# Kernel tuning notes

Hardware: AMD Instinct MI355X
Metric: run time of the kernel (lower is better)

The kernel has to match this reference:

```python
import jax, jax.numpy as jnp
import numpy as np

M = 512          # n_clusters
D_PER = 32       # examples per cluster
FEAT = 1024      # embedding dim
ALPHA = 1.0
N_CLASSES = 128
EPS = 1e-8


def setup_inputs() -> dict:
    key = jax.random.key(0)
    k1, k2 = jax.random.split(key)
    N = M * D_PER
    inp = jax.random.normal(k1, (N, FEAT), dtype=jnp.float32)
    # class label per cluster, repeated d times so each contiguous chunk shares a class
    cluster_classes = jax.random.randint(k2, (M,), 0, N_CLASSES, dtype=jnp.int32)
    target = jnp.repeat(cluster_classes, D_PER)
    return {"input": inp, "target": target}


def reference(input, target):
    N, feat = input.shape
    m, d = M, D_PER
    # cluster assignment: sorted arange(m) repeated d times == repeat(arange(m), d)
    clusters = jnp.repeat(jnp.arange(m), d)                      # [N]
    cluster_classes = target[0 : m * d : d]                      # [m]

    # segment mean over contiguous equal-size chunks (== torch.chunk + mean + stack)
    means = input.reshape(m, d, feat).mean(axis=1)               # [m, feat]

    r2 = jnp.sum(input * input, axis=1, keepdims=True)           # [N,1]
    c2 = jnp.sum(means * means, axis=1)                          # [m]
    sample_costs = r2 + c2[None, :] - 2.0 * (input @ means.T)    # [N, m]

    # distance of each example to its own cluster mean
    intra = jnp.take_along_axis(sample_costs, clusters[:, None], axis=1)[:, 0]  # [N]

    variance = jnp.sum(intra) / float(N - 1)
    var_norm = -1.0 / (2.0 * variance ** 2)

    numerator = jnp.exp(var_norm * intra - ALPHA)                # [N]

    diff_class_mask = (target[:, None] != cluster_classes[None, :]).astype(input.dtype)  # [N,m]
    denominator = jnp.sum(diff_class_mask * jnp.exp(var_norm * sample_costs), axis=1)    # [N]

    losses = jax.nn.relu(-jnp.log(numerator / (denominator + EPS) + EPS))
    total_loss = jnp.mean(losses)

    pred = jnp.argmin(sample_costs, axis=1)                      # [N]
    acc = jnp.mean((pred == clusters).astype(jnp.float32))
    return total_loss, losses, pred, acc
```

## Files before the change

kernel.cpp:

```cpp
#include <hip/hip_runtime.h>
#include <math.h>

#define NCLUST 512
#define DPER 32
#define NFEAT 1024
#define NSAMP (NCLUST * DPER)
#define ALPHA_C 1.0f
#define EPS_C 1e-8f
#define MARGIN_C 0.25f

#define GBM 128
#define GBN 128
#define GBK 64
#define NCHUNK 8

typedef __attribute__((ext_vector_type(4))) float f32x4;
typedef __attribute__((ext_vector_type(8))) _Float16 f16x8;

__device__ __forceinline__ unsigned f2h(float f) {
  _Float16 h = (_Float16)f;
  return (unsigned)__builtin_bit_cast(ushort, h);
}

__device__ __forceinline__ void gload16(const ushort* g, ushort* l) {
  __builtin_amdgcn_global_load_lds(
      (const __attribute__((address_space(1))) unsigned int*)g,
      (__attribute__((address_space(3))) unsigned int*)l, 16, 0, 0);
}

__global__ __launch_bounds__(256) void k_pre(const float* __restrict__ inp,
                                             const int* __restrict__ target,
                                             float* __restrict__ means,
                                             ushort* __restrict__ Bf16,
                                             ushort* __restrict__ Af16,
                                             float* __restrict__ c2,
                                             float* __restrict__ r2g,
                                             float* __restrict__ percl,
                                             int* __restrict__ ccls,
                                             int* __restrict__ wcount) {
  const int m = blockIdx.x;
  const int t = threadIdx.x;
  const int w = t >> 6, l = t & 63;
  __shared__ float ldsm[4][NFEAT];
  __shared__ float red4[4];
  __shared__ float redi[4];

  const float* rowbase = inp + (size_t)m * DPER * NFEAT;
  ushort* arowbase = Af16 + (size_t)m * DPER * NFEAT;

  float4 macc0 = {0,0,0,0}, macc1 = {0,0,0,0}, macc2 = {0,0,0,0}, macc3 = {0,0,0,0};
  float r2keep[8];

  #pragma unroll 2
  for (int rr = 0; rr < 8; ++rr) {
    const int d = w * 8 + rr;
    const float* rp = rowbase + (size_t)d * NFEAT + l * 4;
    const float4 v0 = *(const float4*)(rp);
    const float4 v1 = *(const float4*)(rp + 256);
    const float4 v2 = *(const float4*)(rp + 512);
    const float4 v3 = *(const float4*)(rp + 768);
    ushort* ap = arowbase + (size_t)d * NFEAT + l * 4;
    uint2 h;
    h.x = f2h(v0.x) | (f2h(v0.y) << 16); h.y = f2h(v0.z) | (f2h(v0.w) << 16);
    *(uint2*)(ap) = h;
    h.x = f2h(v1.x) | (f2h(v1.y) << 16); h.y = f2h(v1.z) | (f2h(v1.w) << 16);
    *(uint2*)(ap + 256) = h;
    h.x = f2h(v2.x) | (f2h(v2.y) << 16); h.y = f2h(v2.z) | (f2h(v2.w) << 16);
    *(uint2*)(ap + 512) = h;
    h.x = f2h(v3.x) | (f2h(v3.y) << 16); h.y = f2h(v3.z) | (f2h(v3.w) << 16);
    *(uint2*)(ap + 768) = h;
    macc0.x += v0.x; macc0.y += v0.y; macc0.z += v0.z; macc0.w += v0.w;
    macc1.x += v1.x; macc1.y += v1.y; macc1.z += v1.z; macc1.w += v1.w;
    macc2.x += v2.x; macc2.y += v2.y; macc2.z += v2.z; macc2.w += v2.w;
    macc3.x += v3.x; macc3.y += v3.y; macc3.z += v3.z; macc3.w += v3.w;
    float p = v0.x*v0.x + v0.y*v0.y + v0.z*v0.z + v0.w*v0.w
            + v1.x*v1.x + v1.y*v1.y + v1.z*v1.z + v1.w*v1.w
            + v2.x*v2.x + v2.y*v2.y + v2.z*v2.z + v2.w*v2.w
            + v3.x*v3.x + v3.y*v3.y + v3.z*v3.z + v3.w*v3.w;
    #pragma unroll
    for (int off = 32; off; off >>= 1) p += __shfl_down(p, off);
    r2keep[rr] = p;
  }
  if (l == 0) {
    float r2s = 0.f;
    #pragma unroll
    for (int rr = 0; rr < 8; ++rr) {
      r2g[m * DPER + w * 8 + rr] = r2keep[rr];
      r2s += r2keep[rr];
    }
    redi[w] = r2s;
  }
  *(float4*)&ldsm[w][0 * 256 + l * 4] = macc0;
  *(float4*)&ldsm[w][1 * 256 + l * 4] = macc1;
  *(float4*)&ldsm[w][2 * 256 + l * 4] = macc2;
  *(float4*)&ldsm[w][3 * 256 + l * 4] = macc3;
  __syncthreads();
  float4 s0 = *(const float4*)&ldsm[0][t * 4];
  float4 s1 = *(const float4*)&ldsm[1][t * 4];
  float4 s2 = *(const float4*)&ldsm[2][t * 4];
  float4 s3 = *(const float4*)&ldsm[3][t * 4];
  const float inv = 1.0f / 32.0f;
  float4 mn;
  mn.x = (s0.x + s1.x + s2.x + s3.x) * inv;
  mn.y = (s0.y + s1.y + s2.y + s3.y) * inv;
  mn.z = (s0.z + s1.z + s2.z + s3.z) * inv;
  mn.w = (s0.w + s1.w + s2.w + s3.w) * inv;
  *(float4*)(means + (size_t)m * NFEAT + t * 4) = mn;
  uint2 bw;
  bw.x = f2h(mn.x) | (f2h(mn.y) << 16);
  bw.y = f2h(mn.z) | (f2h(mn.w) << 16);
  *(uint2*)&Bf16[(size_t)m * NFEAT + t * 4] = bw;
  float sq = mn.x * mn.x + mn.y * mn.y + mn.z * mn.z + mn.w * mn.w;
  #pragma unroll
  for (int off = 32; off; off >>= 1) sq += __shfl_down(sq, off);
  if (l == 0) red4[w] = sq;
  __syncthreads();
  if (t == 0) {
    const float cc = red4[0] + red4[1] + red4[2] + red4[3];
    c2[m] = cc;
    ccls[m] = target[m * DPER];
    percl[m] = (redi[0] + redi[1] + redi[2] + redi[3]) - 32.0f * cc;
    if (m == 0) *wcount = 0;
  }
}

__global__ __launch_bounds__(256, 2) void k_gemm(
    const ushort* __restrict__ Af16, const ushort* __restrict__ Bf16,
    const float* __restrict__ c2, const float* __restrict__ r2,
    const float* __restrict__ percl, const int* __restrict__ ccls,
    const int* __restrict__ target,
    float* __restrict__ den_p, float* __restrict__ minv_p,
    float* __restrict__ minv2_p, float* __restrict__ minc_p,
    float* __restrict__ intra_g) {
  __shared__ ushort As[2][GBM * GBK];
  __shared__ ushort Bs[2][GBN * GBK];
  __shared__ float redv[4];
  const int t = threadIdx.x;
  const int l = t & 63, w = t >> 6;
  const int wg = (blockIdx.x & 7) * 64 + (blockIdx.x >> 3);
  const int rowblk = wg >> 2, colblk = wg & 3;
  const int row0 = rowblk * GBM, c0 = colblk * GBN;
  const int wr = w >> 1, wc = w & 1;

  const int sR = l >> 3;
  const int sg = (l & 7) ^ sR;
  const ushort* sA = Af16 + (size_t)(row0 + w * 32 + sR) * NFEAT + sg * 8;
  const ushort* sB = Bf16 + (size_t)(c0 + w * 32 + sR) * NFEAT + sg * 8;

  const int fr = l & 15, fq = l >> 4;
  const int swz = fr & 7;

  f32x4 acc[4][4];
  #pragma unroll
  for (int i = 0; i < 4; ++i)
    #pragma unroll
    for (int j = 0; j < 4; ++j) acc[i][j] = (f32x4){0.f, 0.f, 0.f, 0.f};

#define STAGE(bi, ks) do {                                                   \
    _Pragma("unroll") for (int i = 0; i < 4; ++i)                            \
      gload16(sA + (size_t)i * 8 * NFEAT + (ks) * GBK,                       \
              &As[bi][(w * 32 + i * 8) * GBK]);                              \
    _Pragma("unroll") for (int i = 0; i < 4; ++i)                            \
      gload16(sB + (size_t)i * 8 * NFEAT + (ks) * GBK,                       \
              &Bs[bi][(w * 32 + i * 8) * GBK]);                              \
  } while (0)

#define COMPUTE(bi) do {                                                     \
    _Pragma("unroll") for (int kg = 0; kg < 2; ++kg) {                       \
      const int ch = (((kg * 4 + fq) ^ swz) * 8);                            \
      f16x8 a[4], b[4];                                                      \
      _Pragma("unroll") for (int i = 0; i < 4; ++i)                          \
        a[i] = *(const f16x8*)&As[bi][(wr * 64 + i * 16 + fr) * GBK + ch];   \
      _Pragma("unroll") for (int j = 0; j < 4; ++j)                          \
        b[j] = *(const f16x8*)&Bs[bi][(wc * 64 + j * 16 + fr) * GBK + ch];   \
      _Pragma("unroll") for (int i = 0; i < 4; ++i)                          \
        _Pragma("unroll") for (int j = 0; j < 4; ++j)                        \
          acc[i][j] = __builtin_amdgcn_mfma_f32_16x16x32_f16(a[i], b[j],     \
                                                         acc[i][j], 0,0,0);  \
    }                                                                        \
  } while (0)

  STAGE(0, 0);
  #pragma unroll 1
  for (int ks = 0; ks < NFEAT / GBK - 2; ks += 2) {
    STAGE(1, ks + 1);
    asm volatile("s_waitcnt vmcnt(8)" ::: "memory");
    __builtin_amdgcn_s_barrier();
    COMPUTE(0);
    __builtin_amdgcn_s_barrier();
    STAGE(0, ks + 2);
    asm volatile("s_waitcnt vmcnt(8)" ::: "memory");
    __builtin_amdgcn_s_barrier();
    COMPUTE(1);
    __builtin_amdgcn_s_barrier();
  }
  STAGE(1, NFEAT / GBK - 1);
  asm volatile("s_waitcnt vmcnt(8)" ::: "memory");
  __builtin_amdgcn_s_barrier();
  COMPUTE(0);
  __builtin_amdgcn_s_barrier();
  asm volatile("s_waitcnt vmcnt(0)" ::: "memory");
  __builtin_amdgcn_s_barrier();
  COMPUTE(1);
#undef STAGE
#undef COMPUTE

  float vs = percl[t] + percl[t + 256];
  #pragma unroll
  for (int off = 32; off; off >>= 1) vs += __shfl_down(vs, off);
  if (l == 0) redv[w] = vs;
  __syncthreads();
  const float var = (redv[0] + redv[1] + redv[2] + redv[3]) / (float)(NSAMP - 1);
  const float vn = -1.0f / (2.0f * var * var);

  float c2j[4]; int clsj[4], cjv[4];
  #pragma unroll
  for (int j = 0; j < 4; ++j) {
    const int c = c0 + wc * 64 + j * 16 + fr;
    cjv[j] = c;
    c2j[j] = c2[c];
    clsj[j] = ccls[c];
  }
  const int colchunk = colblk * 2 + wc;
  #pragma unroll
  for (int i = 0; i < 4; ++i) {
    const int rbase = row0 + wr * 64 + i * 16 + fq * 4;
    const int cm = rbase >> 5;
    float r2v[4]; int tg[4];
    #pragma unroll
    for (int v = 0; v < 4; ++v) { r2v[v] = r2[rbase + v]; tg[v] = target[rbase + v]; }
    #pragma unroll
    for (int v = 0; v < 4; ++v) {
      float den = 0.f, bv = 3.4e38f, bv2 = 3.4e38f;
      int bc = 1 << 30;
      #pragma unroll
      for (int j = 0; j < 4; ++j) {
        const float cost = r2v[v] + c2j[j] - 2.0f * acc[i][j][v];
        if (clsj[j] != tg[v]) den += __expf(vn * cost);
        if (cjv[j] == cm) intra_g[rbase + v] = cost;
        if (cost < bv) { bv2 = bv; bv = cost; bc = cjv[j]; }
        else if (cost < bv2) { bv2 = cost; }
      }
      #pragma unroll
      for (int off = 1; off < 16; off <<= 1) {
        den += __shfl_xor(den, off);
        const float ov = __shfl_xor(bv, off);
        const float ov2 = __shfl_xor(bv2, off);
        const int oc = __shfl_xor(bc, off);
        const float nb2 = fminf(fminf(bv2, ov2), fmaxf(bv, ov));
        if (ov < bv || (ov == bv && oc < bc)) { bv = ov; bc = oc; }
        bv2 = nb2;
      }
      if (fr == 0) {
        const int idx = colchunk * NSAMP + rbase + v;
        den_p[idx] = den;
        minv_p[idx] = bv;
        minv2_p[idx] = bv2;
        minc_p[idx] = (float)bc;
      }
    }
  }
}

__global__ __launch_bounds__(256) void k_fin2(const float* __restrict__ den_p,
                                              const float* __restrict__ minv_p,
                                              const float* __restrict__ minv2_p,
                                              const float* __restrict__ minc_p,
                                              const float* __restrict__ intra_g,
                                              const float* __restrict__ percl,
                                              float* __restrict__ losses,
                                              int* __restrict__ wl,
                                              int* __restrict__ wcount,
                                              unsigned long long* __restrict__ slots) {
  __shared__ float redv[4];
  const int t = threadIdx.x;
  float vs = percl[t] + percl[t + 256];
  #pragma unroll
  for (int off = 32; off; off >>= 1) vs += __shfl_down(vs, off);
  if ((t & 63) == 0) redv[t >> 6] = vs;
  __syncthreads();
  const float var = (redv[0] + redv[1] + redv[2] + redv[3]) / (float)(NSAMP - 1);
  const float vn = -1.0f / (2.0f * var * var);

  const int row = blockIdx.x * 256 + t;
  float den = 0.f, bv = 3.4e38f, bv2 = 3.4e38f, bc = 0.f;
  #pragma unroll
  for (int k = 0; k < NCHUNK; ++k) {
    den += den_p[k * NSAMP + row];
    const float v = minv_p[k * NSAMP + row];
    const float v2 = minv2_p[k * NSAMP + row];
    const float c = minc_p[k * NSAMP + row];
    const float nb2 = fminf(fminf(bv2, v2), fmaxf(bv, v));
    if (v < bv) { bv = v; bc = c; }
    bv2 = nb2;
  }
  const float num = expf(vn * intra_g[row] - ALPHA_C);
  const float ratio = num / (den + EPS_C) + EPS_C;
  float loss = -logf(ratio);
  losses[row] = loss > 0.f ? loss : 0.f;
  if (bv2 - bv < MARGIN_C) {
    slots[row] = 0xFFFFFFFFFFFFFFFFULL;
    int i = atomicAdd(wcount, 1);
    wl[i] = row;
  } else {
    slots[row] = ((unsigned long long)__float_as_uint(bv) << 32) | (unsigned)(int)bc;
  }
}

__global__ __launch_bounds__(256) void k_fix(const float* __restrict__ inp,
                                             const float* __restrict__ means,
                                             const float* __restrict__ c2,
                                             const float* __restrict__ r2,
                                             const int* __restrict__ wl,
                                             const int* __restrict__ wcount,
                                             unsigned long long* __restrict__ slots) {
  __shared__ float rbuf[NFEAT];
  const int t = threadIdx.x;
  const int l = t & 63, w = t >> 6;
  const int cnt = *wcount;
  const int chunk = blockIdx.x & 63;
  for (int wi = blockIdx.x >> 6; wi < cnt; wi += gridDim.x >> 6) {
    const int row = wl[wi];
    __syncthreads();
    *(float4*)&rbuf[t * 4] = *(const float4*)(inp + (size_t)row * NFEAT + t * 4);
    __syncthreads();
    float rb[16];
    #pragma unroll
    for (int q = 0; q < 4; ++q) {
      const float4 v = *(const float4*)&rbuf[q * 256 + l * 4];
      rb[q * 4 + 0] = v.x; rb[q * 4 + 1] = v.y;
      rb[q * 4 + 2] = v.z; rb[q * 4 + 3] = v.w;
    }
    const float r2v = r2[row];
    #pragma unroll
    for (int cc = 0; cc < 2; ++cc) {
      const int c = chunk * 8 + w * 2 + cc;
      const float* mp = means + (size_t)c * NFEAT + l * 4;
      float dot = 0.f;
      #pragma unroll
      for (int q = 0; q < 4; ++q) {
        const float4 m4 = *(const float4*)(mp + q * 256);
        dot += m4.x * rb[q * 4 + 0] + m4.y * rb[q * 4 + 1] +
               m4.z * rb[q * 4 + 2] + m4.w * rb[q * 4 + 3];
      }
      #pragma unroll
      for (int off = 32; off; off >>= 1) dot += __shfl_down(dot, off);
      if (l == 0) {
        const float cost = r2v + c2[c] - 2.0f * dot;
        const unsigned long long enc =
            ((unsigned long long)__float_as_uint(cost) << 32) | (unsigned)c;
        atomicMin(&slots[row], enc);
      }
    }
  }
}

__global__ __launch_bounds__(256) void k_final(const float* __restrict__ losses,
                                               const unsigned long long* __restrict__ slots,
                                               float* __restrict__ preds,
                                               float* __restrict__ out) {
  const int t = threadIdx.x;
  float s = 0.f, cnt = 0.f;
  for (int i = t; i < NSAMP; i += 256) {
    s += losses[i];
    const int p = (int)(unsigned)(slots[i] & 0xFFFFFFFFULL);
    preds[i] = (float)p;
    cnt += (p == (i >> 5)) ? 1.f : 0.f;
  }
  __shared__ float redS[4], redC[4];
  #pragma unroll
  for (int off = 32; off > 0; off >>= 1) {
    s += __shfl_down(s, off);
    cnt += __shfl_down(cnt, off);
  }
  if ((t & 63) == 0) { redS[t >> 6] = s; redC[t >> 6] = cnt; }
  __syncthreads();
  if (t == 0) {
    out[0] = (redS[0] + redS[1] + redS[2] + redS[3]) / (float)NSAMP;
    out[1 + 2 * NSAMP] = (redC[0] + redC[1] + redC[2] + redC[3]) / (float)NSAMP;
  }
}

extern "C" void kernel_launch(void* const* d_in, const int* in_sizes, int n_in,
                              void* d_out, int out_size, void* d_ws, size_t ws_size,
                              hipStream_t stream) {
  const float* inp = (const float*)d_in[0];
  const int* target = (const int*)d_in[1];
  float* out = (float*)d_out;

  ushort* Af16 = (ushort*)d_ws;
  ushort* Bf16 = Af16 + (size_t)NSAMP * NFEAT;
  unsigned long long* slots =
      (unsigned long long*)(Bf16 + (size_t)NCLUST * NFEAT);
  float* means = (float*)(slots + NSAMP);
  float* c2 = means + (size_t)NCLUST * NFEAT;
  float* r2 = c2 + NCLUST;
  float* intra_g = r2 + NSAMP;
  float* vn = intra_g + NSAMP;
  float* percl = vn + 1;
  int* ccls = (int*)(percl + NCLUST);
  float* den_p = (float*)(ccls + NCLUST);
  float* minv_p = den_p + NCHUNK * NSAMP;
  float* minv2_p = minv_p + NCHUNK * NSAMP;
  float* minc_p = minv2_p + NCHUNK * NSAMP;
  int* wl = (int*)(minc_p + NCHUNK * NSAMP);
  int* wcount = wl + NSAMP;

  float* losses = out + 1;
  float* preds = out + 1 + NSAMP;

  hipLaunchKernelGGL(k_pre, dim3(NCLUST), dim3(256), 0, stream,
                     inp, target, means, Bf16, Af16, c2, r2, percl, ccls, wcount);
  hipLaunchKernelGGL(k_gemm, dim3(512), dim3(256), 0, stream,
                     Af16, Bf16, c2, r2, percl, ccls, target,
                     den_p, minv_p, minv2_p, minc_p, intra_g);
  hipLaunchKernelGGL(k_fin2, dim3(NSAMP / 256), dim3(256), 0, stream,
                     den_p, minv_p, minv2_p, minc_p, intra_g, percl, losses,
                     wl, wcount, slots);
  hipLaunchKernelGGL(k_fix, dim3(2048), dim3(256), 0, stream,
                     inp, means, c2, r2, wl, wcount, slots);
  hipLaunchKernelGGL(k_final, dim3(1), dim3(256), 0, stream,
                     losses, slots, preds, out);
}
```

Measured before the change: 84.29 us.

## Fuse per-row finalize into GEMM via last-block counter, hoist epilogue loads

After: 97.80 us. +16.0%, slower.

```diff
diff --git a/kernel.cpp b/kernel.cpp
--- a/kernel.cpp
+++ b/kernel.cpp
@@ -37,7 +37,8 @@
                                              float* __restrict__ r2g,
                                              float* __restrict__ percl,
                                              int* __restrict__ ccls,
-                                             int* __restrict__ wcount) {
+                                             int* __restrict__ wcount,
+                                             int* __restrict__ cnt) {
   const int m = blockIdx.x;
   const int t = threadIdx.x;
   const int w = t >> 6, l = t & 63;
@@ -121,6 +122,7 @@
     ccls[m] = target[m * DPER];
     percl[m] = (redi[0] + redi[1] + redi[2] + redi[3]) - 32.0f * cc;
     if (m == 0) *wcount = 0;
+    if (m < NSAMP / GBM) cnt[m] = 0;
   }
 }
 
@@ -131,10 +133,13 @@
     const int* __restrict__ target,
     float* __restrict__ den_p, float* __restrict__ minv_p,
     float* __restrict__ minv2_p, float* __restrict__ minc_p,
-    float* __restrict__ intra_g) {
+    float* __restrict__ intra_g, float* __restrict__ losses,
+    int* __restrict__ wl, int* __restrict__ wcount,
+    unsigned long long* __restrict__ slots, int* __restrict__ cnt) {
   __shared__ ushort As[2][GBM * GBK];
   __shared__ ushort Bs[2][GBN * GBK];
   __shared__ float redv[4];
+  __shared__ int lastf;
   const int t = threadIdx.x;
   const int l = t & 63, w = t >> 6;
   const int wg = (blockIdx.x & 7) * 64 + (blockIdx.x >> 3);
@@ -149,6 +154,29 @@
 
   const int fr = l & 15, fq = l >> 4;
   const int swz = fr & 7;
+
+  float vs = percl[t] + percl[t + 256];
+  #pragma unroll
+  for (int off = 32; off; off >>= 1) vs += __shfl_down(vs, off);
+  if (l == 0) redv[w] = vs;
+  float c2j[4]; int clsj[4], cjv[4];
+  #pragma unroll
+  for (int j = 0; j < 4; ++j) {
+    const int c = c0 + wc * 64 + j * 16 + fr;
+    cjv[j] = c;
+    c2j[j] = c2[c];
+    clsj[j] = ccls[c];
+  }
+  float r2v[4][4]; int tg[4][4];
+  #pragma unroll
+  for (int i = 0; i < 4; ++i) {
+    const int rbase = row0 + wr * 64 + i * 16 + fq * 4;
+    #pragma unroll
+    for (int v = 0; v < 4; ++v) { r2v[i][v] = r2[rbase + v]; tg[i][v] = target[rbase + v]; }
+  }
+  __syncthreads();
+  const float var = (redv[0] + redv[1] + redv[2] + redv[3]) / (float)(NSAMP - 1);
+  const float vn = -1.0f / (2.0f * var * var);
 
   f32x4 acc[4][4];
   #pragma unroll
@@ -205,38 +233,19 @@
 #undef STAGE
 #undef COMPUTE
 
-  float vs = percl[t] + percl[t + 256];
-  #pragma unroll
-  for (int off = 32; off; off >>= 1) vs += __shfl_down(vs, off);
-  if (l == 0) redv[w] = vs;
-  __syncthreads();
-  const float var = (redv[0] + redv[1] + redv[2] + redv[3]) / (float)(NSAMP - 1);
-  const float vn = -1.0f / (2.0f * var * var);
-
-  float c2j[4]; int clsj[4], cjv[4];
-  #pragma unroll
-  for (int j = 0; j < 4; ++j) {
-    const int c = c0 + wc * 64 + j * 16 + fr;
-    cjv[j] = c;
-    c2j[j] = c2[c];
-    clsj[j] = ccls[c];
-  }
   const int colchunk = colblk * 2 + wc;
   #pragma unroll
   for (int i = 0; i < 4; ++i) {
     const int rbase = row0 + wr * 64 + i * 16 + fq * 4;
     const int cm = rbase >> 5;
-    float r2v[4]; int tg[4];
-    #pragma unroll
-    for (int v = 0; v < 4; ++v) { r2v[v] = r2[rbase + v]; tg[v] = target[rbase + v]; }
     #pragma unroll
     for (int v = 0; v < 4; ++v) {
       float den = 0.f, bv = 3.4e38f, bv2 = 3.4e38f;
       int bc = 1 << 30;
       #pragma unroll
       for (int j = 0; j < 4; ++j) {
-        const float cost = r2v[v] + c2j[j] - 2.0f * acc[i][j][v];
-        if (clsj[j] != tg[v]) den += __expf(vn * cost);
+        const float cost = r2v[i][v] + c2j[j] - 2.0f * acc[i][j][v];
+        if (clsj[j] != tg[i][v]) den += __expf(vn * cost);
         if (cjv[j] == cm) intra_g[rbase + v] = cost;
         if (cost < bv) { bv2 = bv; bv = cost; bc = cjv[j]; }
         else if (cost < bv2) { bv2 = cost; }
@@ -260,50 +269,41 @@
       }
     }
   }
-}
-
-__global__ __launch_bounds__(256) void k_fin2(const float* __restrict__ den_p,
-                                              const float* __restrict__ minv_p,
-                                              const float* __restrict__ minv2_p,
-                                              const float* __restrict__ minc_p,
-                                              const float* __restrict__ intra_g,
-                                              const float* __restrict__ percl,
-                                              float* __restrict__ losses,
-                                              int* __restrict__ wl,
-                                              int* __restrict__ wcount,
-                                              unsigned long long* __restrict__ slots) {
-  __shared__ float redv[4];
-  const int t = threadIdx.x;
-  float vs = percl[t] + percl[t + 256];
-  #pragma unroll
-  for (int off = 32; off; off >>= 1) vs += __shfl_down(vs, off);
-  if ((t & 63) == 0) redv[t >> 6] = vs;
-  __syncthreads();
-  const float var = (redv[0] + redv[1] + redv[2] + redv[3]) / (float)(NSAMP - 1);
-  const float vn = -1.0f / (2.0f * var * var);
-
-  const int row = blockIdx.x * 256 + t;
-  float den = 0.f, bv = 3.4e38f, bv2 = 3.4e38f, bc = 0.f;
-  #pragma unroll
-  for (int k = 0; k < NCHUNK; ++k) {
-    den += den_p[k * NSAMP + row];
-    const float v = minv_p[k * NSAMP + row];
-    const float v2 = minv2_p[k * NSAMP + row];
-    const float c = minc_p[k * NSAMP + row];
-    const float nb2 = fminf(fminf(bv2, v2), fmaxf(bv, v));
-    if (v < bv) { bv = v; bc = c; }
-    bv2 = nb2;
-  }
-  const float num = expf(vn * intra_g[row] - ALPHA_C);
-  const float ratio = num / (den + EPS_C) + EPS_C;
-  float loss = -logf(ratio);
-  losses[row] = loss > 0.f ? loss : 0.f;
-  if (bv2 - bv < MARGIN_C) {
-    slots[row] = 0xFFFFFFFFFFFFFFFFULL;
-    int i = atomicAdd(wcount, 1);
-    wl[i] = row;
-  } else {
-    slots[row] = ((unsigned long long)__float_as_uint(bv) << 32) | (unsigned)(int)bc;
+
+  __syncthreads();
+  if (t == 0) {
+    __threadfence();
+    lastf = (atomicAdd(&cnt[rowblk], 1) == 3);
+  }
+  __syncthreads();
+  if (lastf) {
+    if (t == 0) __threadfence();
+    __syncthreads();
+    if (t < GBM) {
+      const int row = row0 + t;
+      float den = 0.f, bv = 3.4e38f, bv2 = 3.4e38f, bc = 0.f;
+      #pragma unroll
+      for (int k = 0; k < NCHUNK; ++k) {
+        den += den_p[k * NSAMP + row];
+        const float v = minv_p[k * NSAMP + row];
+        const float v2 = minv2_p[k * NSAMP + row];
+        const float c = minc_p[k * NSAMP + row];
+        const float nb2 = fminf(fminf(bv2, v2), fmaxf(bv, v));
+        if (v < bv) { bv = v; bc = c; }
+        bv2 = nb2;
+      }
+      const float num = expf(vn * intra_g[row] - ALPHA_C);
+      const float ratio = num / (den + EPS_C) + EPS_C;
+      float loss = -logf(ratio);
+      losses[row] = loss > 0.f ? loss : 0.f;
+      if (bv2 - bv < MARGIN_C) {
+        slots[row] = 0xFFFFFFFFFFFFFFFFULL;
+        int i = atomicAdd(wcount, 1);
+        wl[i] = row;
+      } else {
+        slots[row] = ((unsigned long long)__float_as_uint(bv) << 32) | (unsigned)(int)bc;
+      }
+    }
   }
 }
 
@@ -331,7 +331,7 @@
       rb[q * 4 + 0] = v.x; rb[q * 4 + 1] = v.y;
       rb[q * 4 + 2] = v.z; rb[q * 4 + 3] = v.w;
     }
-    const float r2v = r2[row];
+    const float r2vv = r2[row];
     #pragma unroll
     for (int cc = 0; cc < 2; ++cc) {
       const int c = chunk * 8 + w * 2 + cc;
@@ -346,7 +346,7 @@
       #pragma unroll
       for (int off = 32; off; off >>= 1) dot += __shfl_down(dot, off);
       if (l == 0) {
-        const float cost = r2v + c2[c] - 2.0f * dot;
+        const float cost = r2vv + c2[c] - 2.0f * dot;
         const unsigned long long enc =
             ((unsigned long long)__float_as_uint(cost) << 32) | (unsigned)c;
         atomicMin(&slots[row], enc);
@@ -405,18 +405,18 @@
   float* minc_p = minv2_p + NCHUNK * NSAMP;
   int* wl = (int*)(minc_p + NCHUNK * NSAMP);
   int* wcount = wl + NSAMP;
+  int* cnt = wcount + 1;
 
   float* losses = out + 1;
   float* preds = out + 1 + NSAMP;
 
   hipLaunchKernelGGL(k_pre, dim3(NCLUST), dim3(256), 0, stream,
-                     inp, target, means, Bf16, Af16, c2, r2, percl, ccls, wcount);
+                     inp, target, means, Bf16, Af16, c2, r2, percl, ccls,
+                     wcount, cnt);
   hipLaunchKernelGGL(k_gemm, dim3(512), dim3(256), 0, stream,
                      Af16, Bf16, c2, r2, percl, ccls, target,
-                     den_p, minv_p, minv2_p, minc_p, intra_g);
-  hipLaunchKernelGGL(k_fin2, dim3(NSAMP / 256), dim3(256), 0, stream,
-                     den_p, minv_p, minv2_p, minc_p, intra_g, percl, losses,
-                     wl, wcount, slots);
+                     den_p, minv_p, minv2_p, minc_p, intra_g,
+                     losses, wl, wcount, slots, cnt);
   hipLaunchKernelGGL(k_fix, dim3(2048), dim3(256), 0, stream,
                      inp, means, c2, r2, wl, wcount, slots);
   hipLaunchKernelGGL(k_final, dim3(1), dim3(256), 0, stream,
```
